# Kernel tuning notes

Measured on AMD Instinct MI355X. Metric: run time of the kernel, lower is better.

## Reference

```python
import jax, jax.numpy as jnp
import numpy as np


def setup_inputs() -> dict:
    key = jax.random.key(0)
    k1, k2, k3 = jax.random.split(key, 3)
    N, C_in, H, W = 32, 64, 128, 128
    C_out, K = 128, 3
    fan_in = C_in * K * K
    bound = 1.0 / np.sqrt(fan_in)
    x = jax.random.normal(k1, (N, C_in, H, W), dtype=jnp.float32)
    weight = jax.random.uniform(k2, (C_out, C_in, K, K), dtype=jnp.float32, minval=-bound, maxval=bound)
    bias = jax.random.uniform(k3, (C_out,), dtype=jnp.float32, minval=-bound, maxval=bound)
    return {"x": x, "weight": weight, "bias": bias}


def reference(x, weight, bias):
    # conv2d, stride=1, padding=0 (VALID), NCHW / OIHW
    y = jax.lax.conv_general_dilated(
        x, weight,
        window_strides=(1, 1),
        padding='VALID',
        dimension_numbers=('NCHW', 'OIHW', 'NCHW'),
    )
    y = y + bias[None, :, None, None]          # [N, C_out, H_out, W_out]
    y = jnp.min(y, axis=1, keepdims=True)      # channel-wise min -> [N, 1, H_out, W_out]
    return jnp.tanh(jnp.tanh(y))
```

## Files before the change

### kernel.cpp

```cpp
#include <hip/hip_runtime.h>
#include <hip/hip_bf16.h>

typedef __attribute__((ext_vector_type(8))) short short8_t;
typedef __attribute__((ext_vector_type(4))) float floatx4;
typedef unsigned short ushort_t;
typedef unsigned int uint_t;

#define TILE_B 16896

#define RSTR 72
#define TSZ  (132 * RSTR)

__device__ __forceinline__ uint_t rne_u(float f) {
    uint_t u = __float_as_uint(f);
    return u + (0x7fffu + ((u >> 16) & 1u));
}
__device__ __forceinline__ uint_t pk2(float lo, float hi) {
    return __builtin_amdgcn_perm(rne_u(hi), rne_u(lo), 0x07060302u);
}

__global__ __launch_bounds__(256)
void prepass_fused(const float* __restrict__ x, const float* __restrict__ w,
                   ushort_t* __restrict__ x2, ushort_t* __restrict__ w2)
{
    __shared__ __align__(16) float lds[64 * 129];
    const int t = threadIdx.x;
    const int b = blockIdx.x;
    if (b >= 4096) {
        int idx = (b - 4096) * 256 + t;
        int rd  = idx >> 12;
        int rem = idx & 4095;
        int co  = rem >> 5;
        int c32 = rem & 31;
        int khw = rd >> 1, half = rd & 1;
        int ci  = half * 32 + c32;
        w2[idx] = (ushort_t)(rne_u(w[co * 576 + ci * 9 + khw]) >> 16);
        return;
    }
    const int n = b >> 7, h = b & 127;
    const float* xp = x + ((size_t)n << 20) + (size_t)h * 128;
#pragma unroll
    for (int r = 0; r < 16; ++r) {
        int flat = r * 256 + t;
        int ci = flat >> 6, wh = flat & 63;
        float2 v = *reinterpret_cast<const float2*>(xp + (size_t)ci * 16384 + wh * 2);
        lds[ci * 129 + wh * 2]     = v.x;
        lds[ci * 129 + wh * 2 + 1] = v.y;
    }
    __syncthreads();
    ushort_t* op = x2 + ((size_t)n * 128 + h) * 8192;
#pragma unroll
    for (int r = 0; r < 4; ++r) {
        int id = r * 256 + t;
        int wq = id >> 3, q = id & 7;
        uint_t o[4];
#pragma unroll
        for (int qq = 0; qq < 4; ++qq)
            o[qq] = pk2(lds[(q * 8 + 2 * qq) * 129 + wq],
                        lds[(q * 8 + 2 * qq + 1) * 129 + wq]);
        *reinterpret_cast<uint4*>(op + (size_t)wq * 64 + q * 8) =
            make_uint4(o[0], o[1], o[2], o[3]);
    }
}

__global__ __launch_bounds__(512, 4)
void conv_v7(const ushort_t* __restrict__ x2, const ushort_t* __restrict__ w2,
             const float* __restrict__ bias, float* __restrict__ out)
{
    __shared__ __align__(16) ushort_t T[4 * (TILE_B / 2)];
    __shared__ __align__(16) float red[2][256];

    const int tid  = threadIdx.x;
    const int bid0 = blockIdx.x;
    const int bid  = (bid0 & 7) * 252 + (bid0 >> 3);
    const int n    = bid / 63;
    const int ho0  = (bid - n * 63) * 2;

    const int lane = tid & 63;
    const int wid  = tid >> 6;
    const int wm   = wid >> 1;
    const int wn   = wid & 1;
    const int r16  = lane & 15;
    const int quad = lane >> 4;

    const int voffB = ((lane >> 3) * 128) + (((lane & 7) ^ (lane >> 3)) * 16);
    const ushort_t* xrow = x2 + ((size_t)n * 128 + ho0) * 8192;
#pragma unroll
    for (int s = 0; s < 4; ++s)
#pragma unroll
        for (int k = 0; k < 2; ++k) {
            const int col0 = (wid * 2 + k) * 8;
            const char* g = (const char*)xrow + (size_t)s * 16384 + col0 * 128 + voffB;
            const ushort_t* l = &T[(s * TILE_B + col0 * 128) / 2];
            __builtin_amdgcn_global_load_lds(
                (const __attribute__((address_space(1))) uint_t*)g,
                (__attribute__((address_space(3))) uint_t*)l, 16, 0, 0);
        }

    {
        const int s = tid >> 7, rem = tid & 127;
        reinterpret_cast<uint_t*>(T)[(s * TILE_B + (128 + (rem >> 5)) * 128) / 4 + (rem & 31)] = 0u;
    }

    floatx4 acc[4][4];
#pragma unroll
    for (int i = 0; i < 4; ++i)
#pragma unroll
        for (int j = 0; j < 4; ++j)
            acc[i][j] = (floatx4){0.f, 0.f, 0.f, 0.f};

    const ushort_t* w2base = w2 + (size_t)(wn * 64 + r16) * 32 + quad * 8;

    const int mc0 = (wm & 1) * 64 + r16;
    const int ms0 = wm >> 1;

    short8_t bcur[4], bnxt[4];
#pragma unroll
    for (int t4 = 0; t4 < 4; ++t4)
        bcur[t4] = *reinterpret_cast<const short8_t*>(w2base + t4 * 512);

    __syncthreads();

#pragma unroll
    for (int rd = 0; rd < 18; ++rd) {
        if (rd < 17) {
            const ushort_t* bb = w2base + (rd + 1) * 4096;
#pragma unroll
            for (int t4 = 0; t4 < 4; ++t4)
                bnxt[t4] = *reinterpret_cast<const short8_t*>(bb + t4 * 512);
        }

        const int khw  = rd >> 1;
        const int kh   = khw / 3;
        const int kw   = khw - kh * 3;
        const int half = rd & 1;

        short8_t afr[4];
        {
            const int c0 = mc0 + kw;
            const int abase = (ms0 + kh) * TILE_B + c0 * 128
                            + (((half * 4 + quad) ^ (c0 & 7)) * 16);
            const char* ap = (const char*)T + abase;
#pragma unroll
            for (int t4 = 0; t4 < 4; ++t4)
                afr[t4] = *reinterpret_cast<const short8_t*>(ap + t4 * 2048);
        }

#pragma unroll
        for (int tm = 0; tm < 4; ++tm)
#pragma unroll
            for (int tn = 0; tn < 4; ++tn)
                acc[tm][tn] = __builtin_amdgcn_mfma_f32_16x16x32_bf16(
                    afr[tm], bcur[tn], acc[tm][tn], 0, 0, 0);

#pragma unroll
        for (int t4 = 0; t4 < 4; ++t4)
            bcur[t4] = bnxt[t4];
    }

    float bvv[4];
#pragma unroll
    for (int tn = 0; tn < 4; ++tn)
        bvv[tn] = bias[wn * 64 + tn * 16 + r16];

#pragma unroll
    for (int tm = 0; tm < 4; ++tm) {
#pragma unroll
        for (int r = 0; r < 4; ++r) {
            float v = acc[tm][0][r] + bvv[0];
            v = fminf(v, acc[tm][1][r] + bvv[1]);
            v = fminf(v, acc[tm][2][r] + bvv[2]);
            v = fminf(v, acc[tm][3][r] + bvv[3]);
            v = fminf(v, __shfl_xor(v, 1, 64));
            v = fminf(v, __shfl_xor(v, 2, 64));
            v = fminf(v, __shfl_xor(v, 4, 64));
            v = fminf(v, __shfl_xor(v, 8, 64));
            if (r16 == 0)
                red[wn][wm * 64 + tm * 16 + quad * 4 + r] = v;
        }
    }
    __syncthreads();

    if (tid < 256) {
        const int r  = tid >> 7;
        const int wo = tid & 127;
        if (wo < 126) {
            float v = fminf(red[0][tid], red[1][tid]);
            v = tanhf(tanhf(v));
            out[((size_t)n * 126 + ho0 + r) * 126 + wo] = v;
        }
    }
}

__global__ void w2_prepass(const float* __restrict__ w, ushort_t* __restrict__ w2) {
    int idx = blockIdx.x * 256 + threadIdx.x;
    int rd  = idx >> 12;
    int rem = idx & 4095;
    int co  = rem >> 5;
    int c32 = rem & 31;
    int khw = rd >> 1, half = rd & 1;
    int ci  = half * 32 + c32;
    w2[idx] = (ushort_t)(rne_u(w[co * 576 + ci * 9 + khw]) >> 16);
}

template<bool USE_W2>
__global__ __launch_bounds__(512, 4)
void conv_min_tanh_kernel(const float* __restrict__ x,
                          const float* __restrict__ w,
                          const ushort_t* __restrict__ w2,
                          const float* __restrict__ bias,
                          float* __restrict__ out)
{
    __shared__ __align__(16) ushort_t T[4 * TSZ];
    __shared__ __align__(16) float red[2][256];

    const int tid  = threadIdx.x;
    const int bid0 = blockIdx.x;
    const int bid  = (bid0 & 7) * 252 + (bid0 >> 3);
    const int n    = bid / 63;
    const int ho0  = (bid - n * 63) * 2;

    const int tx = tid & 31;
    const int ty = tid >> 5;

    const int lane = tid & 63;
    const int wid  = tid >> 6;
    const int wm   = wid >> 1;
    const int wn   = wid & 1;
    const int r16  = lane & 15;
    const int quad = lane >> 4;

    const float* xbase = x + ((size_t)n << 20) + (size_t)ho0 * 128;

    auto load_row = [&](floatx4 (&dv)[4], const int s) {
#pragma unroll
        for (int j = 0; j < 4; ++j)
            dv[j] = *reinterpret_cast<const floatx4*>(
                xbase + (size_t)(ty * 4 + j) * 16384 + s * 128 + tx * 4);
    };
    auto conv_row = [&](floatx4 (&dv)[4], const int s) {
#pragma unroll
        for (int i = 0; i < 4; ++i) {
            uint2 u;
            u.x = pk2(dv[0][i], dv[1][i]);
            u.y = pk2(dv[2][i], dv[3][i]);
            const int c   = tx * 4 + i;
            const int swz = (ty >> 1) ^ ((c >> 3) & 7);
            *reinterpret_cast<uint2*>(&T[s * TSZ + c * RSTR + swz * 8 + (ty & 1) * 4]) = u;
        }
    };

    floatx4 dva[4], dvb[4];
    load_row(dva, 0);
    load_row(dvb, 1);

    for (int idx = tid; idx < 576; idx += 512) {
        int s = idx / 144, o = idx - s * 144;
        reinterpret_cast<uint_t*>(T)[s * (TSZ / 2) + (128 * RSTR) / 2 + o] = 0u;
    }

    conv_row(dva, 0);
    load_row(dva, 2);
    conv_row(dvb, 1);
    load_row(dvb, 3);
    conv_row(dva, 2);
    conv_row(dvb, 3);

    floatx4 acc[4][4];
#pragma unroll
    for (int i = 0; i < 4; ++i)
#pragma unroll
        for (int j = 0; j < 4; ++j)
            acc[i][j] = (floatx4){0.f, 0.f, 0.f, 0.f};

    const ushort_t* w2base = w2 + (size_t)(wn * 64 + r16) * 32 + quad * 8;
    const float*    wbase  = w + (size_t)(wn * 64 + r16) * 576;

    __syncthreads();

#pragma unroll
    for (int rd = 0; rd < 18; ++rd) {
        const int khw  = rd >> 1;
        const int kh   = khw / 3;
        const int kw   = khw - kh * 3;
        const int half = rd & 1;

        short8_t bfr[4];
        if (USE_W2) {
            const ushort_t* bb = w2base + rd * 4096;
#pragma unroll
            for (int t4 = 0; t4 < 4; ++t4)
                bfr[t4] = *reinterpret_cast<const short8_t*>(bb + t4 * 512);
        } else {
#pragma unroll
            for (int t4 = 0; t4 < 4; ++t4) {
                const float* wp = wbase + (size_t)t4 * (16 * 576)
                                + (size_t)(half * 32 + quad * 8) * 9 + khw;
                short8_t b;
#pragma unroll
                for (int q = 0; q < 4; ++q) {
                    uint_t u = pk2(wp[(2 * q) * 9], wp[(2 * q + 1) * 9]);
                    b[2 * q]     = (short)(u & 0xffffu);
                    b[2 * q + 1] = (short)(u >> 16);
                }
                bfr[t4] = b;
            }
        }

        short8_t afr[4];
#pragma unroll
        for (int t4 = 0; t4 < 4; ++t4) {
            const int m  = wm * 64 + t4 * 16 + r16;
            const int s  = (m >> 7) + kh;
            const int c  = (m & 127) + kw;
            const int sw = (half * 4 + quad) ^ ((c >> 3) & 7);
            afr[t4] = *reinterpret_cast<const short8_t*>(&T[s * TSZ + c * RSTR + sw * 8]);
        }
#pragma unroll
        for (int tm = 0; tm < 4; ++tm)
#pragma unroll
            for (int tn = 0; tn < 4; ++tn)
                acc[tm][tn] = __builtin_amdgcn_mfma_f32_16x16x32_bf16(
                    afr[tm], bfr[tn], acc[tm][tn], 0, 0, 0);
    }

    float bvv[4];
#pragma unroll
    for (int tn = 0; tn < 4; ++tn)
        bvv[tn] = bias[wn * 64 + tn * 16 + r16];

#pragma unroll
    for (int tm = 0; tm < 4; ++tm) {
#pragma unroll
        for (int r = 0; r < 4; ++r) {
            float v = acc[tm][0][r] + bvv[0];
            v = fminf(v, acc[tm][1][r] + bvv[1]);
            v = fminf(v, acc[tm][2][r] + bvv[2]);
            v = fminf(v, acc[tm][3][r] + bvv[3]);
            v = fminf(v, __shfl_xor(v, 1, 64));
            v = fminf(v, __shfl_xor(v, 2, 64));
            v = fminf(v, __shfl_xor(v, 4, 64));
            v = fminf(v, __shfl_xor(v, 8, 64));
            if (r16 == 0)
                red[wn][wm * 64 + tm * 16 + quad * 4 + r] = v;
        }
    }
    __syncthreads();

    if (tid < 256) {
        const int r  = tid >> 7;
        const int wo = tid & 127;
        if (wo < 126) {
            float v = fminf(red[0][tid], red[1][tid]);
            v = tanhf(tanhf(v));
            out[((size_t)n * 126 + ho0 + r) * 126 + wo] = v;
        }
    }
}

extern "C" void kernel_launch(void* const* d_in, const int* in_sizes, int n_in,
                              void* d_out, int out_size, void* d_ws, size_t ws_size,
                              hipStream_t stream) {
    const float* x    = (const float*)d_in[0];
    const float* w    = (const float*)d_in[1];
    const float* bias = (const float*)d_in[2];
    float* out = (float*)d_out;

    const size_t X2B = (size_t)32 * 128 * 128 * 64 * 2;
    const size_t W2B = (size_t)73728 * 2;

    if (ws_size >= X2B + W2B) {
        ushort_t* x2 = (ushort_t*)d_ws;
        ushort_t* w2 = (ushort_t*)((char*)d_ws + X2B);
        prepass_fused<<<dim3(4096 + 288), dim3(256), 0, stream>>>(x, w, x2, w2);
        conv_v7<<<dim3(2016), dim3(512), 0, stream>>>(x2, w2, bias, out);
    } else if (ws_size >= W2B) {
        ushort_t* w2 = (ushort_t*)d_ws;
        w2_prepass<<<dim3(288), dim3(256), 0, stream>>>(w, w2);
        conv_min_tanh_kernel<true><<<dim3(2016), dim3(512), 0, stream>>>(x, w, w2, bias, out);
    } else {
        conv_min_tanh_kernel<false><<<dim3(2016), dim3(512), 0, stream>>>(x, w, nullptr, bias, out);
    }
}
```

Baseline: 276.3 us.

## Halve conv block to 4 waves with 8x4 MFMA tiles per wave; widen prepass loads

The main conv kernel now runs 256 threads (4 waves) per block instead of 512, and each wave computes 8 M-tiles by 4 N-tiles instead of 4x4. This doubles per-wave reuse of the B fragments and reduces redundant weight loads across waves, at the cost of twice the accumulator registers and lower occupancy (launch bounds 256,2). The prepass transposition also switches from float2 to float4 global loads to cut the number of load instructions.

Result: faster. 268.9 us (-2.7%).

```diff
diff --git a/kernel.cpp b/kernel.cpp
--- a/kernel.cpp
+++ b/kernel.cpp
@@ -40,12 +40,14 @@
     const int n = b >> 7, h = b & 127;
     const float* xp = x + ((size_t)n << 20) + (size_t)h * 128;
 #pragma unroll
-    for (int r = 0; r < 16; ++r) {
+    for (int r = 0; r < 8; ++r) {
         int flat = r * 256 + t;
-        int ci = flat >> 6, wh = flat & 63;
-        float2 v = *reinterpret_cast<const float2*>(xp + (size_t)ci * 16384 + wh * 2);
-        lds[ci * 129 + wh * 2]     = v.x;
-        lds[ci * 129 + wh * 2 + 1] = v.y;
+        int ci = flat >> 5, wq = flat & 31;
+        float4 v = *reinterpret_cast<const float4*>(xp + (size_t)ci * 16384 + wq * 4);
+        lds[ci * 129 + wq * 4 + 0] = v.x;
+        lds[ci * 129 + wq * 4 + 1] = v.y;
+        lds[ci * 129 + wq * 4 + 2] = v.z;
+        lds[ci * 129 + wq * 4 + 3] = v.w;
     }
     __syncthreads();
     ushort_t* op = x2 + ((size_t)n * 128 + h) * 8192;
@@ -63,8 +65,8 @@
     }
 }
 
-__global__ __launch_bounds__(512, 4)
-void conv_v7(const ushort_t* __restrict__ x2, const ushort_t* __restrict__ w2,
+__global__ __launch_bounds__(256, 2)
+void conv_v8(const ushort_t* __restrict__ x2, const ushort_t* __restrict__ w2,
              const float* __restrict__ bias, float* __restrict__ out)
 {
     __shared__ __align__(16) ushort_t T[4 * (TILE_B / 2)];
@@ -88,8 +90,8 @@
 #pragma unroll
     for (int s = 0; s < 4; ++s)
 #pragma unroll
-        for (int k = 0; k < 2; ++k) {
-            const int col0 = (wid * 2 + k) * 8;
+        for (int k = 0; k < 4; ++k) {
+            const int col0 = (wid * 4 + k) * 8;
             const char* g = (const char*)xrow + (size_t)s * 16384 + col0 * 128 + voffB;
             const ushort_t* l = &T[(s * TILE_B + col0 * 128) / 2];
             __builtin_amdgcn_global_load_lds(
@@ -97,27 +99,26 @@
                 (__attribute__((address_space(3))) uint_t*)l, 16, 0, 0);
         }
 
-    {
-        const int s = tid >> 7, rem = tid & 127;
+#pragma unroll
+    for (int it = 0; it < 2; ++it) {
+        const int idx = it * 256 + tid;
+        const int s = idx >> 7, rem = idx & 127;
         reinterpret_cast<uint_t*>(T)[(s * TILE_B + (128 + (rem >> 5)) * 128) / 4 + (rem & 31)] = 0u;
     }
 
-    floatx4 acc[4][4];
-#pragma unroll
-    for (int i = 0; i < 4; ++i)
+    floatx4 acc[8][4];
+#pragma unroll
+    for (int i = 0; i < 8; ++i)
 #pragma unroll
         for (int j = 0; j < 4; ++j)
             acc[i][j] = (floatx4){0.f, 0.f, 0.f, 0.f};
 
     const ushort_t* w2base = w2 + (size_t)(wn * 64 + r16) * 32 + quad * 8;
 
-    const int mc0 = (wm & 1) * 64 + r16;
-    const int ms0 = wm >> 1;
-
     short8_t bcur[4], bnxt[4];
 #pragma unroll
-    for (int t4 = 0; t4 < 4; ++t4)
-        bcur[t4] = *reinterpret_cast<const short8_t*>(w2base + t4 * 512);
+    for (int tn = 0; tn < 4; ++tn)
+        bcur[tn] = *reinterpret_cast<const short8_t*>(w2base + tn * 512);
 
     __syncthreads();
 
@@ -126,8 +127,8 @@
         if (rd < 17) {
             const ushort_t* bb = w2base + (rd + 1) * 4096;
 #pragma unroll
-            for (int t4 = 0; t4 < 4; ++t4)
-                bnxt[t4] = *reinterpret_cast<const short8_t*>(bb + t4 * 512);
+            for (int tn = 0; tn < 4; ++tn)
+                bnxt[tn] = *reinterpret_cast<const short8_t*>(bb + tn * 512);
         }
 
         const int khw  = rd >> 1;
@@ -135,27 +136,193 @@
         const int kw   = khw - kh * 3;
         const int half = rd & 1;
 
-        short8_t afr[4];
+        short8_t afr[8];
         {
-            const int c0 = mc0 + kw;
-            const int abase = (ms0 + kh) * TILE_B + c0 * 128
+            const int c0 = r16 + kw;
+            const int abase = (wm + kh) * TILE_B + c0 * 128
                             + (((half * 4 + quad) ^ (c0 & 7)) * 16);
             const char* ap = (const char*)T + abase;
 #pragma unroll
-            for (int t4 = 0; t4 < 4; ++t4)
-                afr[t4] = *reinterpret_cast<const short8_t*>(ap + t4 * 2048);
-        }
-
-#pragma unroll
-        for (int tm = 0; tm < 4; ++tm)
+            for (int tm = 0; tm < 8; ++tm)
+                afr[tm] = *reinterpret_cast<const short8_t*>(ap + tm * 2048);
+        }
+
+#pragma unroll
+        for (int tm = 0; tm < 8; ++tm)
 #pragma unroll
             for (int tn = 0; tn < 4; ++tn)
                 acc[tm][tn] = __builtin_amdgcn_mfma_f32_16x16x32_bf16(
                     afr[tm], bcur[tn], acc[tm][tn], 0, 0, 0);
 
 #pragma unroll
-        for (int t4 = 0; t4 < 4; ++t4)
-            bcur[t4] = bnxt[t4];
+        for (int tn = 0; tn < 4; ++tn)
+            bcur[tn] = bnxt[tn];
+    }
+
+    float bvv[4];
+#pragma unroll
+    for (int tn = 0; tn < 4; ++tn)
+        bvv[tn] = bias[wn * 64 + tn * 16 + r16];
+
+#pragma unroll
+    for (int tm = 0; tm < 8; ++tm) {
+#pragma unroll
+        for (int r = 0; r < 4; ++r) {
+            float v = acc[tm][0][r] + bvv[0];
+            v = fminf(v, acc[tm][1][r] + bvv[1]);
+            v = fminf(v, acc[tm][2][r] + bvv[2]);
+            v = fminf(v, acc[tm][3][r] + bvv[3]);
+            v = fminf(v, __shfl_xor(v, 1, 64));
+            v = fminf(v, __shfl_xor(v, 2, 64));
+            v = fminf(v, __shfl_xor(v, 4, 64));
+            v = fminf(v, __shfl_xor(v, 8, 64));
+            if (r16 == 0)
+                red[wn][wm * 128 + tm * 16 + quad * 4 + r] = v;
+        }
+    }
+    __syncthreads();
+
+    {
+        const int r  = tid >> 7;
+        const int wo = tid & 127;
+        if (wo < 126) {
+            float v = fminf(red[0][tid], red[1][tid]);
+            v = tanhf(tanhf(v));
+            out[((size_t)n * 126 + ho0 + r) * 126 + wo] = v;
+        }
+    }
+}
+
+__global__ void w2_prepass(const float* __restrict__ w, ushort_t* __restrict__ w2) {
+    int idx = blockIdx.x * 256 + threadIdx.x;
+    int rd  = idx >> 12;
+    int rem = idx & 4095;
+    int co  = rem >> 5;
+    int c32 = rem & 31;
+    int khw = rd >> 1, half = rd & 1;
+    int ci  = half * 32 + c32;
+    w2[idx] = (ushort_t)(rne_u(w[co * 576 + ci * 9 + khw]) >> 16);
+}
+
+template<bool USE_W2>
+__global__ __launch_bounds__(512, 4)
+void conv_min_tanh_kernel(const float* __restrict__ x,
+                          const float* __restrict__ w,
+                          const ushort_t* __restrict__ w2,
+                          const float* __restrict__ bias,
+                          float* __restrict__ out)
+{
+    __shared__ __align__(16) ushort_t T[4 * TSZ];
+    __shared__ __align__(16) float red[2][256];
+
+    const int tid  = threadIdx.x;
+    const int bid0 = blockIdx.x;
+    const int bid  = (bid0 & 7) * 252 + (bid0 >> 3);
+    const int n    = bid / 63;
+    const int ho0  = (bid - n * 63) * 2;
+
+    const int tx = tid & 31;
+    const int ty = tid >> 5;
+
+    const int lane = tid & 63;
+    const int wid  = tid >> 6;
+    const int wm   = wid >> 1;
+    const int wn   = wid & 1;
+    const int r16  = lane & 15;
+    const int quad = lane >> 4;
+
+    const float* xbase = x + ((size_t)n << 20) + (size_t)ho0 * 128;
+
+    auto load_row = [&](floatx4 (&dv)[4], const int s) {
+#pragma unroll
+        for (int j = 0; j < 4; ++j)
+            dv[j] = *reinterpret_cast<const floatx4*>(
+                xbase + (size_t)(ty * 4 + j) * 16384 + s * 128 + tx * 4);
+    };
+    auto conv_row = [&](floatx4 (&dv)[4], const int s) {
+#pragma unroll
+        for (int i = 0; i < 4; ++i) {
+            uint2 u;
+            u.x = pk2(dv[0][i], dv[1][i]);
+            u.y = pk2(dv[2][i], dv[3][i]);
+            const int c   = tx * 4 + i;
+            const int swz = (ty >> 1) ^ ((c >> 3) & 7);
+            *reinterpret_cast<uint2*>(&T[s * TSZ + c * RSTR + swz * 8 + (ty & 1) * 4]) = u;
+        }
+    };
+
+    floatx4 dva[4], dvb[4];
+    load_row(dva, 0);
+    load_row(dvb, 1);
+
+    for (int idx = tid; idx < 576; idx += 512) {
+        int s = idx / 144, o = idx - s * 144;
+        reinterpret_cast<uint_t*>(T)[s * (TSZ / 2) + (128 * RSTR) / 2 + o] = 0u;
+    }
+
+    conv_row(dva, 0);
+    load_row(dva, 2);
+    conv_row(dvb, 1);
+    load_row(dvb, 3);
+    conv_row(dva, 2);
+    conv_row(dvb, 3);
+
+    floatx4 acc[4][4];
+#pragma unroll
+    for (int i = 0; i < 4; ++i)
+#pragma unroll
+        for (int j = 0; j < 4; ++j)
+            acc[i][j] = (floatx4){0.f, 0.f, 0.f, 0.f};
+
+    const ushort_t* w2base = w2 + (size_t)(wn * 64 + r16) * 32 + quad * 8;
+    const float*    wbase  = w + (size_t)(wn * 64 + r16) * 576;
+
+    __syncthreads();
+
+#pragma unroll
+    for (int rd = 0; rd < 18; ++rd) {
+        const int khw  = rd >> 1;
+        const int kh   = khw / 3;
+        const int kw   = khw - kh * 3;
+        const int half = rd & 1;
+
+        short8_t bfr[4];
+        if (USE_W2) {
+            const ushort_t* bb = w2base + rd * 4096;
+#pragma unroll
+            for (int t4 = 0; t4 < 4; ++t4)
+                bfr[t4] = *reinterpret_cast<const short8_t*>(bb + t4 * 512);
+        } else {
+#pragma unroll
+            for (int t4 = 0; t4 < 4; ++t4) {
+                const float* wp = wbase + (size_t)t4 * (16 * 576)
+                                + (size_t)(half * 32 + quad * 8) * 9 + khw;
+                short8_t b;
+#pragma unroll
+                for (int q = 0; q < 4; ++q) {
+                    uint_t u = pk2(wp[(2 * q) * 9], wp[(2 * q + 1) * 9]);
+                    b[2 * q]     = (short)(u & 0xffffu);
+                    b[2 * q + 1] = (short)(u >> 16);
+                }
+                bfr[t4] = b;
+            }
+        }
+
+        short8_t afr[4];
+#pragma unroll
+        for (int t4 = 0; t4 < 4; ++t4) {
+            const int m  = wm * 64 + t4 * 16 + r16;
+            const int s  = (m >> 7) + kh;
+            const int c  = (m & 127) + kw;
+            const int sw = (half * 4 + quad) ^ ((c >> 3) & 7);
+            afr[t4] = *reinterpret_cast<const short8_t*>(&T[s * TSZ + c * RSTR + sw * 8]);
+        }
+#pragma unroll
+        for (int tm = 0; tm < 4; ++tm)
+#pragma unroll
+            for (int tn = 0; tn < 4; ++tn)
+                acc[tm][tn] = __builtin_amdgcn_mfma_f32_16x16x32_bf16(
+                    afr[tm], bfr[tn], acc[tm][tn], 0, 0, 0);
     }
 
     float bvv[4];
@@ -192,172 +359,6 @@
     }
 }
 
-__global__ void w2_prepass(const float* __restrict__ w, ushort_t* __restrict__ w2) {
-    int idx = blockIdx.x * 256 + threadIdx.x;
-    int rd  = idx >> 12;
-    int rem = idx & 4095;
-    int co  = rem >> 5;
-    int c32 = rem & 31;
-    int khw = rd >> 1, half = rd & 1;
-    int ci  = half * 32 + c32;
-    w2[idx] = (ushort_t)(rne_u(w[co * 576 + ci * 9 + khw]) >> 16);
-}
-
-template<bool USE_W2>
-__global__ __launch_bounds__(512, 4)
-void conv_min_tanh_kernel(const float* __restrict__ x,
-                          const float* __restrict__ w,
-                          const ushort_t* __restrict__ w2,
-                          const float* __restrict__ bias,
-                          float* __restrict__ out)
-{
-    __shared__ __align__(16) ushort_t T[4 * TSZ];
-    __shared__ __align__(16) float red[2][256];
-
-    const int tid  = threadIdx.x;
-    const int bid0 = blockIdx.x;
-    const int bid  = (bid0 & 7) * 252 + (bid0 >> 3);
-    const int n    = bid / 63;
-    const int ho0  = (bid - n * 63) * 2;
-
-    const int tx = tid & 31;
-    const int ty = tid >> 5;
-
-    const int lane = tid & 63;
-    const int wid  = tid >> 6;
-    const int wm   = wid >> 1;
-    const int wn   = wid & 1;
-    const int r16  = lane & 15;
-    const int quad = lane >> 4;
-
-    const float* xbase = x + ((size_t)n << 20) + (size_t)ho0 * 128;
-
-    auto load_row = [&](floatx4 (&dv)[4], const int s) {
-#pragma unroll
-        for (int j = 0; j < 4; ++j)
-            dv[j] = *reinterpret_cast<const floatx4*>(
-                xbase + (size_t)(ty * 4 + j) * 16384 + s * 128 + tx * 4);
-    };
-    auto conv_row = [&](floatx4 (&dv)[4], const int s) {
-#pragma unroll
-        for (int i = 0; i < 4; ++i) {
-            uint2 u;
-            u.x = pk2(dv[0][i], dv[1][i]);
-            u.y = pk2(dv[2][i], dv[3][i]);
-            const int c   = tx * 4 + i;
-            const int swz = (ty >> 1) ^ ((c >> 3) & 7);
-            *reinterpret_cast<uint2*>(&T[s * TSZ + c * RSTR + swz * 8 + (ty & 1) * 4]) = u;
-        }
-    };
-
-    floatx4 dva[4], dvb[4];
-    load_row(dva, 0);
-    load_row(dvb, 1);
-
-    for (int idx = tid; idx < 576; idx += 512) {
-        int s = idx / 144, o = idx - s * 144;
-        reinterpret_cast<uint_t*>(T)[s * (TSZ / 2) + (128 * RSTR) / 2 + o] = 0u;
-    }
-
-    conv_row(dva, 0);
-    load_row(dva, 2);
-    conv_row(dvb, 1);
-    load_row(dvb, 3);
-    conv_row(dva, 2);
-    conv_row(dvb, 3);
-
-    floatx4 acc[4][4];
-#pragma unroll
-    for (int i = 0; i < 4; ++i)
-#pragma unroll
-        for (int j = 0; j < 4; ++j)
-            acc[i][j] = (floatx4){0.f, 0.f, 0.f, 0.f};
-
-    const ushort_t* w2base = w2 + (size_t)(wn * 64 + r16) * 32 + quad * 8;
-    const float*    wbase  = w + (size_t)(wn * 64 + r16) * 576;
-
-    __syncthreads();
-
-#pragma unroll
-    for (int rd = 0; rd < 18; ++rd) {
-        const int khw  = rd >> 1;
-        const int kh   = khw / 3;
-        const int kw   = khw - kh * 3;
-        const int half = rd & 1;
-
-        short8_t bfr[4];
-        if (USE_W2) {
-            const ushort_t* bb = w2base + rd * 4096;
-#pragma unroll
-            for (int t4 = 0; t4 < 4; ++t4)
-                bfr[t4] = *reinterpret_cast<const short8_t*>(bb + t4 * 512);
-        } else {
-#pragma unroll
-            for (int t4 = 0; t4 < 4; ++t4) {
-                const float* wp = wbase + (size_t)t4 * (16 * 576)
-                                + (size_t)(half * 32 + quad * 8) * 9 + khw;
-                short8_t b;
-#pragma unroll
-                for (int q = 0; q < 4; ++q) {
-                    uint_t u = pk2(wp[(2 * q) * 9], wp[(2 * q + 1) * 9]);
-                    b[2 * q]     = (short)(u & 0xffffu);
-                    b[2 * q + 1] = (short)(u >> 16);
-                }
-                bfr[t4] = b;
-            }
-        }
-
-        short8_t afr[4];
-#pragma unroll
-        for (int t4 = 0; t4 < 4; ++t4) {
-            const int m  = wm * 64 + t4 * 16 + r16;
-            const int s  = (m >> 7) + kh;
-            const int c  = (m & 127) + kw;
-            const int sw = (half * 4 + quad) ^ ((c >> 3) & 7);
-            afr[t4] = *reinterpret_cast<const short8_t*>(&T[s * TSZ + c * RSTR + sw * 8]);
-        }
-#pragma unroll
-        for (int tm = 0; tm < 4; ++tm)
-#pragma unroll
-            for (int tn = 0; tn < 4; ++tn)
-                acc[tm][tn] = __builtin_amdgcn_mfma_f32_16x16x32_bf16(
-                    afr[tm], bfr[tn], acc[tm][tn], 0, 0, 0);
-    }
-
-    float bvv[4];
-#pragma unroll
-    for (int tn = 0; tn < 4; ++tn)
-        bvv[tn] = bias[wn * 64 + tn * 16 + r16];
-
-#pragma unroll
-    for (int tm = 0; tm < 4; ++tm) {
-#pragma unroll
-        for (int r = 0; r < 4; ++r) {
-            float v = acc[tm][0][r] + bvv[0];
-            v = fminf(v, acc[tm][1][r] + bvv[1]);
-            v = fminf(v, acc[tm][2][r] + bvv[2]);
-            v = fminf(v, acc[tm][3][r] + bvv[3]);
-            v = fminf(v, __shfl_xor(v, 1, 64));
-            v = fminf(v, __shfl_xor(v, 2, 64));
-            v = fminf(v, __shfl_xor(v, 4, 64));
-            v = fminf(v, __shfl_xor(v, 8, 64));
-            if (r16 == 0)
-                red[wn][wm * 64 + tm * 16 + quad * 4 + r] = v;
-        }
-    }
-    __syncthreads();
-
-    if (tid < 256) {
-        const int r  = tid >> 7;
-        const int wo = tid & 127;
-        if (wo < 126) {
-            float v = fminf(red[0][tid], red[1][tid]);
-            v = tanhf(tanhf(v));
-            out[((size_t)n * 126 + ho0 + r) * 126 + wo] = v;
-        }
-    }
-}
-
 extern "C" void kernel_launch(void* const* d_in, const int* in_sizes, int n_in,
                               void* d_out, int out_size, void* d_ws, size_t ws_size,
                               hipStream_t stream) {
@@ -373,7 +374,7 @@
         ushort_t* x2 = (ushort_t*)d_ws;
         ushort_t* w2 = (ushort_t*)((char*)d_ws + X2B);
         prepass_fused<<<dim3(4096 + 288), dim3(256), 0, stream>>>(x, w, x2, w2);
-        conv_v7<<<dim3(2016), dim3(512), 0, stream>>>(x2, w2, bias, out);
+        conv_v8<<<dim3(2016), dim3(256), 0, stream>>>(x2, w2, bias, out);
     } else if (ws_size >= W2B) {
         ushort_t* w2 = (ushort_t*)d_ws;
         w2_prepass<<<dim3(288), dim3(256), 0, stream>>>(w, w2);
```
